# Optimization experiments

Hardware: AMD Instinct MI355X
Metric: run time of the kernel (lower is better)

Reference implementation:

```python
import jax, jax.numpy as jnp
import numpy as np

D_MODEL = 512
D_INNER = 1024   # expand * d_model
D_STATE = 16
D_CONV = 4
DT_RANK = 32     # ceil(d_model / 16)
N_LAYERS = 4
N_PRED_LAYERS = 2
FEAT = 128
LN_EPS = 1e-5


def _ln(x, w, b):
    m = x.mean(-1, keepdims=True)
    v = ((x - m) ** 2).mean(-1, keepdims=True)
    return (x - m) * jax.lax.rsqrt(v + LN_EPS) * w + b


def _silu(x):
    return x * jax.nn.sigmoid(x)


def _causal_conv(x, w, b):
    # depthwise causal conv1d: x (B,L,C), w (C,K), b (C,)
    K = w.shape[1]
    L = x.shape[1]
    xp = jnp.pad(x, ((0, 0), (K - 1, 0), (0, 0)))
    y = b
    for k in range(K):
        y = y + xp[:, k:k + L, :] * w[:, k]
    return y


def _mamba(x, in_w, conv_w, conv_b, xp_w, dt_w, dt_b, Alog, Dp, out_w):
    # x: (B,L,d_model)
    xz = jnp.einsum('bld,ed->ble', x, in_w)          # (B,L,2*d_inner)
    xi, z = jnp.split(xz, 2, axis=-1)
    xc = _silu(_causal_conv(xi, conv_w, conv_b))     # (B,L,d_inner)
    dbc = jnp.einsum('blc,ec->ble', xc, xp_w)        # (B,L,dt_rank+2N)
    dt = dbc[..., :DT_RANK]
    Bm = dbc[..., DT_RANK:DT_RANK + D_STATE]         # (B,L,N)
    Cm = dbc[..., DT_RANK + D_STATE:]                # (B,L,N)
    delta = jax.nn.softplus(jnp.einsum('blr,cr->blc', dt, dt_w) + dt_b)  # (B,L,d_inner)
    A = -jnp.exp(Alog)                               # (d_inner,N), negative
    dA = jnp.exp(delta[..., None] * A)               # (B,L,d_inner,N)
    dBu = delta[..., None] * Bm[:, :, None, :] * xc[..., None]

    def step(h, inp):
        dA_t, dBu_t, C_t = inp
        h = dA_t * h + dBu_t                         # (B,d_inner,N)
        y = jnp.einsum('bcn,bn->bc', h, C_t)
        return h, y

    h0 = jnp.zeros((x.shape[0], D_INNER, D_STATE), x.dtype)
    _, ys = jax.lax.scan(step, h0, (dA.transpose(1, 0, 2, 3),
                                    dBu.transpose(1, 0, 2, 3),
                                    Cm.transpose(1, 0, 2)))
    y = ys.transpose(1, 0, 2) + Dp * xc              # skip connection D*u
    y = y * _silu(z)
    return jnp.einsum('blc,dc->bld', y, out_w)


def _forward(x, inp_w, inp_b, enc_ln_w, enc_ln_b, enc_in_w, enc_conv_w, enc_conv_b,
             enc_xp_w, enc_dt_w, enc_dt_b, enc_Alog, enc_D, enc_out_w,
             fin_ln_w, fin_ln_b, prd_ln_w, prd_ln_b, prd_in_w, prd_conv_w, prd_conv_b,
             prd_xp_w, prd_dt_w, prd_dt_b, prd_Alog, prd_D, prd_out_w,
             prd_nrm_w, prd_nrm_b, prd_proj_w, prd_proj_b):
    # MambaEncoder: input_proj + n_layers pre-norm residual Mamba blocks + final LN
    h = jnp.einsum('blf,df->bld', x, inp_w) + inp_b
    for i in range(N_LAYERS):
        h = h + _mamba(_ln(h, enc_ln_w[i], enc_ln_b[i]),
                       enc_in_w[i], enc_conv_w[i], enc_conv_b[i], enc_xp_w[i],
                       enc_dt_w[i], enc_dt_b[i], enc_Alog[i], enc_D[i], enc_out_w[i])
    ctx = _ln(h, fin_ln_w, fin_ln_b)
    # MambaPredictor: small causal mamba stack + norm + proj
    p = ctx
    for i in range(N_PRED_LAYERS):
        p = p + _mamba(_ln(p, prd_ln_w[i], prd_ln_b[i]),
                       prd_in_w[i], prd_conv_w[i], prd_conv_b[i], prd_xp_w[i],
                       prd_dt_w[i], prd_dt_b[i], prd_Alog[i], prd_D[i], prd_out_w[i])
    p = _ln(p, prd_nrm_w, prd_nrm_b)
    preds = jnp.einsum('bld,ed->ble', p, prd_proj_w) + prd_proj_b
    return preds


def _mamba_params(key, n, scale=0.02):
    ks = jax.random.split(key, 6)
    arange_A = jnp.tile(jnp.log(jnp.arange(1, D_STATE + 1, dtype=jnp.float32)), (n, D_INNER, 1))
    return dict(
        in_w=jax.random.normal(ks[0], (n, 2 * D_INNER, D_MODEL)) * scale,
        conv_w=jax.random.normal(ks[1], (n, D_INNER, D_CONV)) * scale,
        conv_b=jnp.zeros((n, D_INNER)),
        xp_w=jax.random.normal(ks[2], (n, DT_RANK + 2 * D_STATE, D_INNER)) * scale,
        dt_w=jax.random.normal(ks[3], (n, D_INNER, DT_RANK)) * scale,
        dt_b=jnp.full((n, D_INNER), jnp.log(jnp.expm1(0.01))),  # inv-softplus(0.01)
        Alog=arange_A,
        D=jnp.ones((n, D_INNER)),
        out_w=jax.random.normal(ks[4], (n, D_MODEL, D_INNER)) * scale,
    )


def setup_inputs() -> dict:
    key = jax.random.key(0)
    ks = jax.random.split(key, 8)
    enc = _mamba_params(ks[0], N_LAYERS)
    prd = _mamba_params(ks[1], N_PRED_LAYERS)
    return {
        'x': jax.random.normal(ks[2], (2, 1024, FEAT), dtype=jnp.float32),
        'inp_w': jax.random.normal(ks[3], (D_MODEL, FEAT)) * 0.02,
        'inp_b': jnp.zeros((D_MODEL,)),
        'enc_ln_w': jnp.ones((N_LAYERS, D_MODEL)), 'enc_ln_b': jnp.zeros((N_LAYERS, D_MODEL)),
        'enc_in_w': enc['in_w'], 'enc_conv_w': enc['conv_w'], 'enc_conv_b': enc['conv_b'],
        'enc_xp_w': enc['xp_w'], 'enc_dt_w': enc['dt_w'], 'enc_dt_b': enc['dt_b'],
        'enc_Alog': enc['Alog'], 'enc_D': enc['D'], 'enc_out_w': enc['out_w'],
        'fin_ln_w': jnp.ones((D_MODEL,)), 'fin_ln_b': jnp.zeros((D_MODEL,)),
        'prd_ln_w': jnp.ones((N_PRED_LAYERS, D_MODEL)), 'prd_ln_b': jnp.zeros((N_PRED_LAYERS, D_MODEL)),
        'prd_in_w': prd['in_w'], 'prd_conv_w': prd['conv_w'], 'prd_conv_b': prd['conv_b'],
        'prd_xp_w': prd['xp_w'], 'prd_dt_w': prd['dt_w'], 'prd_dt_b': prd['dt_b'],
        'prd_Alog': prd['Alog'], 'prd_D': prd['D'], 'prd_out_w': prd['out_w'],
        'prd_nrm_w': jnp.ones((D_MODEL,)), 'prd_nrm_b': jnp.zeros((D_MODEL,)),
        'prd_proj_w': jax.random.normal(ks[4], (D_MODEL, D_MODEL)) * 0.02,
        'prd_proj_b': jnp.zeros((D_MODEL,)),
    }


def reference(x, inp_w, inp_b, enc_ln_w, enc_ln_b, enc_in_w, enc_conv_w, enc_conv_b,
              enc_xp_w, enc_dt_w, enc_dt_b, enc_Alog, enc_D, enc_out_w,
              fin_ln_w, fin_ln_b, prd_ln_w, prd_ln_b, prd_in_w, prd_conv_w, prd_conv_b,
              prd_xp_w, prd_dt_w, prd_dt_b, prd_Alog, prd_D, prd_out_w,
              prd_nrm_w, prd_nrm_b, prd_proj_w, prd_proj_b):
    return _forward(x, inp_w, inp_b, enc_ln_w, enc_ln_b, enc_in_w, enc_conv_w, enc_conv_b,
                    enc_xp_w, enc_dt_w, enc_dt_b, enc_Alog, enc_D, enc_out_w,
                    fin_ln_w, fin_ln_b, prd_ln_w, prd_ln_b, prd_in_w, prd_conv_w, prd_conv_b,
                    prd_xp_w, prd_dt_w, prd_dt_b, prd_Alog, prd_D, prd_out_w,
                    prd_nrm_w, prd_nrm_b, prd_proj_w, prd_proj_b)
```

## Files before the change

kernel.cpp:

```cpp
#include <hip/hip_runtime.h>
#include <hip/hip_bf16.h>

using bf16 = __hip_bfloat16;
typedef __attribute__((ext_vector_type(8))) short short8;
typedef __attribute__((ext_vector_type(4))) float f32x4;

static constexpr int LB = 2;
static constexpr int LL = 1024;
static constexpr int DM = 512;
static constexpr int DI = 1024;
static constexpr int DSN = 16;
static constexpr int RK = 32;
static constexpr int MR_ROWS = LB * LL;

static constexpr int NCHUNK = 64;
static constexpr int CH = LL / NCHUNK;

__device__ __forceinline__ void gload16(const void* g, void* l) {
    __builtin_amdgcn_global_load_lds(
        (__attribute__((address_space(1))) void*)(g),
        (__attribute__((address_space(3))) void*)(l), 16, 0, 0);
}

struct ConvArgs {
    const float* src[9];
    bf16*        dst[9];
    int          n4[9];
};

__global__ __launch_bounds__(256) void convert_bf16_multi(ConvArgs a) {
    const int s = blockIdx.y;
    const float4* __restrict__ src = (const float4*)a.src[s];
    bf16* __restrict__ dst = a.dst[s];
    const int n4 = a.n4[s];
    for (int i = blockIdx.x * 256 + threadIdx.x; i < n4; i += gridDim.x * 256) {
        float4 v = src[i];
        bf16 t[4] = {__float2bfloat16(v.x), __float2bfloat16(v.y),
                     __float2bfloat16(v.z), __float2bfloat16(v.w)};
        *(uint2*)(dst + (size_t)i * 4) = *(uint2*)t;
    }
}

__global__ __launch_bounds__(256) void transpose_dtw(const float* __restrict__ enc_dtw,
                                                     const float* __restrict__ prd_dtw,
                                                     float* __restrict__ out) {
    const int layer = blockIdx.y;
    const float* src = (layer < 4) ? enc_dtw + (size_t)layer * DI * RK
                                   : prd_dtw + (size_t)(layer - 4) * DI * RK;
    float* dst = out + (size_t)layer * RK * DI;
    const int idx = blockIdx.x * 256 + threadIdx.x;
    const int k = idx >> 10, c = idx & (DI - 1);
    dst[idx] = src[(size_t)c * RK + k];
}

__device__ __forceinline__ void ln_store(float* outrow, int tid, float a, float b) {
    ((float2*)outrow)[tid] = make_float2(a, b);
}
__device__ __forceinline__ void ln_store(bf16* outrow, int tid, float a, float b) {
    __hip_bfloat162 h;
    h.x = __float2bfloat16(a);
    h.y = __float2bfloat16(b);
    ((__hip_bfloat162*)outrow)[tid] = h;
}

template <typename T>
__global__ __launch_bounds__(256) void ln_kernel(const float* __restrict__ x,
                                                 const float* __restrict__ w,
                                                 const float* __restrict__ b,
                                                 T* __restrict__ out) {
    const int row = blockIdx.x;
    const int tid = threadIdx.x;
    const int wid = tid >> 6, lane = tid & 63;
    __shared__ float red[8];

    const float2 v = ((const float2*)(x + (size_t)row * DM))[tid];
    float s = v.x + v.y;
#pragma unroll
    for (int m = 1; m < 64; m <<= 1) s += __shfl_xor(s, m);
    if (lane == 0) red[wid] = s;
    __syncthreads();
    const float mean = (red[0] + red[1] + red[2] + red[3]) * (1.f / DM);
    const float d0 = v.x - mean, d1 = v.y - mean;
    float s2 = d0 * d0 + d1 * d1;
#pragma unroll
    for (int m = 1; m < 64; m <<= 1) s2 += __shfl_xor(s2, m);
    if (lane == 0) red[4 + wid] = s2;
    __syncthreads();
    const float var = (red[4] + red[5] + red[6] + red[7]) * (1.f / DM);
    const float rs = rsqrtf(var + 1e-5f);
    const float2 wv = ((const float2*)w)[tid];
    const float2 bv = ((const float2*)b)[tid];
    ln_store(out + (size_t)row * DM, tid, d0 * rs * wv.x + bv.x, d1 * rs * wv.y + bv.y);
}

template <int BM, int BN, int BK, int EPI>
__global__ __launch_bounds__(256) void gemm_bt(const bf16* __restrict__ A, int lda,
                                               const bf16* __restrict__ B, int ldb,
                                               float* __restrict__ C, int ldc,
                                               int K, const float* __restrict__ bias) {
    static_assert(BK == 64, "layout assumes 128B LDS row");
    static_assert(BM % 32 == 0 && BN % 32 == 0, "wave staging granularity");
    constexpr int MR = (BM / 2) / 16;
    constexpr int NR = (BN / 2) / 16;
    __shared__ __align__(16) char sA[BM * 128];
    __shared__ __align__(16) char sB[BN * 128];

    const int tid = threadIdx.x;
    const int lane = tid & 63, wid = tid >> 6;
    const int wr = wid >> 1, wc = wid & 1;
    const int m0 = blockIdx.y * BM, n0 = blockIdx.x * BN;
    const int kbase = (EPI == 2) ? blockIdx.z * K : 0;

    f32x4 acc[MR][NR] = {};

    const int lrow = lane >> 3;
    const int lcol = (lane & 7) ^ lrow;
    const size_t lda2 = (size_t)lda * 2, ldb2 = (size_t)ldb * 2;
    const char* Ab = (const char*)A + (size_t)(m0 + wid * (BM / 4) + lrow) * lda2
                     + lcol * 16 + (size_t)kbase * 2;
    const char* Bb = (const char*)B + (size_t)(n0 + wid * (BN / 4) + lrow) * ldb2
                     + lcol * 16 + (size_t)kbase * 2;
    char* sAw = sA + wid * (BM / 4) * 128;
    char* sBw = sB + wid * (BN / 4) * 128;

    for (int k0 = 0; k0 < K; k0 += BK) {
#pragma unroll
        for (int i = 0; i < BM / 32; ++i)
            gload16(Ab + (size_t)i * 8 * lda2 + (size_t)k0 * 2, sAw + i * 1024);
#pragma unroll
        for (int i = 0; i < BN / 32; ++i)
            gload16(Bb + (size_t)i * 8 * ldb2 + (size_t)k0 * 2, sBw + i * 1024);
        __syncthreads();
#pragma unroll
        for (int kk = 0; kk < BK; kk += 32) {
            const int kb2 = (kk + (lane >> 4) * 8) * 2;
            short8 af[MR], bfr[NR];
#pragma unroll
            for (int m = 0; m < MR; ++m) {
                const int r = wr * (BM / 2) + m * 16 + (lane & 15);
                af[m] = *(const short8*)(sA + r * 128 + (kb2 ^ ((r & 7) << 4)));
            }
#pragma unroll
            for (int n = 0; n < NR; ++n) {
                const int r = wc * (BN / 2) + n * 16 + (lane & 15);
                bfr[n] = *(const short8*)(sB + r * 128 + (kb2 ^ ((r & 7) << 4)));
            }
#pragma unroll
            for (int m = 0; m < MR; ++m) {
#pragma unroll
                for (int n = 0; n < NR; ++n) {
                    acc[m][n] = __builtin_amdgcn_mfma_f32_16x16x32_bf16(af[m], bfr[n], acc[m][n], 0, 0, 0);
                }
            }
        }
        __syncthreads();
    }

#pragma unroll
    for (int m = 0; m < MR; ++m) {
#pragma unroll
        for (int n = 0; n < NR; ++n) {
            const int col = n0 + wc * (BN / 2) + n * 16 + (lane & 15);
            const float bv = (EPI == 1) ? bias[col] : 0.f;
#pragma unroll
            for (int j = 0; j < 4; ++j) {
                const int row = m0 + wr * (BM / 2) + m * 16 + (lane >> 4) * 4 + j;
                float v = acc[m][n][j] + bv;
                float* p = C + (size_t)row * ldc + col;
                if (EPI == 2) {
                    atomicAdd(p, v);
                } else {
                    if (EPI == 3) v += *p;
                    *p = v;
                }
            }
        }
    }
}

__global__ __launch_bounds__(256) void conv_silu_kernel(const float* __restrict__ xz,
                                                        const float* __restrict__ cw,
                                                        const float* __restrict__ cb,
                                                        float* __restrict__ xc,
                                                        bf16* __restrict__ xc_bf,
                                                        float* __restrict__ dbc_zero) {
    if (blockIdx.x < 128) {
        ((float4*)dbc_zero)[blockIdx.x * 256 + threadIdx.x] = make_float4(0.f, 0.f, 0.f, 0.f);
    }
    const int idx = blockIdx.x * 256 + threadIdx.x;
    const int c = idx & (DI - 1);
    const int r = idx >> 10;
    const int l = r & (LL - 1);
    const float* xi = xz + (size_t)r * (2 * DI) + c;
    const float4 w = *(const float4*)(cw + (size_t)c * 4);
    float acc = cb[c] + w.w * xi[0];
    if (l >= 1) acc += w.z * xi[-(2 * DI)];
    if (l >= 2) acc += w.y * xi[-(4 * DI)];
    if (l >= 3) acc += w.x * xi[-(6 * DI)];
    const float s = acc / (1.f + expf(-acc));
    xc[idx] = s;
    xc_bf[idx] = __float2bfloat16(s);
}

__global__ __launch_bounds__(256) void scan_part1(const float* __restrict__ xc,
                                                  const float* __restrict__ dbc,
                                                  const float* __restrict__ Alog,
                                                  const float* __restrict__ dtw_t,
                                                  const float* __restrict__ dtb,
                                                  float* __restrict__ delta,
                                                  float* __restrict__ psum,
                                                  float* __restrict__ ssum) {
    const int lane = threadIdx.x & 63;
    const int wsub = threadIdx.x >> 6;
    const int c = blockIdx.x * 64 + lane;
    const int chunk = blockIdx.y * 4 + wsub;
    const int b = blockIdx.z;
    const int r0 = b * LL + chunk * CH;

    float wv[RK];
#pragma unroll
    for (int k = 0; k < RK; ++k) wv[k] = dtw_t[(size_t)k * DI + c];
    const float bdt = dtb[c];

    float a2[DSN];
#pragma unroll
    for (int q = 0; q < 4; ++q) {
        const float4 al = *(const float4*)(Alog + (size_t)c * DSN + q * 4);
        a2[q * 4 + 0] = -expf(al.x) * 1.44269504f;
        a2[q * 4 + 1] = -expf(al.y) * 1.44269504f;
        a2[q * 4 + 2] = -expf(al.z) * 1.44269504f;
        a2[q * 4 + 3] = -expf(al.w) * 1.44269504f;
    }

    float h[DSN], P[DSN];
#pragma unroll
    for (int n = 0; n < DSN; ++n) { h[n] = 0.f; P[n] = 1.f; }

    for (int t = 0; t < CH; ++t) {
        const size_t r = r0 + t;
        float acc = bdt;
#pragma unroll
        for (int q = 0; q < RK / 4; ++q) {
            const float4 d4 = *(const float4*)(dbc + r * 64 + q * 4);
            acc = fmaf(d4.x, wv[q * 4 + 0], acc);
            acc = fmaf(d4.y, wv[q * 4 + 1], acc);
            acc = fmaf(d4.z, wv[q * 4 + 2], acc);
            acc = fmaf(d4.w, wv[q * 4 + 3], acc);
        }
        const float d = (acc > 20.f) ? acc : log1pf(expf(acc));
        delta[r * DI + c] = d;

        const float xv = xc[r * DI + c];
        const float dxv = d * xv;
        float Bv[DSN];
#pragma unroll
        for (int q = 0; q < 4; ++q)
            *(float4*)&Bv[q * 4] = *(const float4*)(dbc + r * 64 + 32 + q * 4);
#pragma unroll
        for (int n = 0; n < DSN; ++n) {
            const float dA = exp2f(d * a2[n]);
            h[n] = fmaf(dA, h[n], dxv * Bv[n]);
            P[n] *= dA;
        }
    }

    const size_t obase = ((size_t)(b * NCHUNK + chunk) * DSN) * DI + c;
#pragma unroll
    for (int n = 0; n < DSN; ++n) {
        psum[obase + (size_t)n * DI] = P[n];
        ssum[obase + (size_t)n * DI] = h[n];
    }
}

__global__ __launch_bounds__(256) void scan_combine(float* __restrict__ psum,
                                                    const float* __restrict__ ssum) {
    const int lane = threadIdx.x & 63;
    const int idx = blockIdx.y * 4 + (threadIdx.x >> 6);
    const int b = idx >> 4, n = idx & 15;
    const int c = blockIdx.x * 64 + lane;
    const size_t base = ((size_t)(b * NCHUNK) * DSN + n) * DI + c;
    const size_t stride = (size_t)DSN * DI;

    float h = 0.f;
    for (int j0 = 0; j0 < NCHUNK; j0 += 8) {
        float Pv[8], Sv[8];
#pragma unroll
        for (int u = 0; u < 8; ++u) {
            Pv[u] = psum[base + (j0 + u) * stride];
            Sv[u] = ssum[base + (j0 + u) * stride];
        }
#pragma unroll
        for (int u = 0; u < 8; ++u) {
            psum[base + (j0 + u) * stride] = h;
            h = fmaf(Pv[u], h, Sv[u]);
        }
    }
}

__global__ __launch_bounds__(256) void scan_part3(const float* __restrict__ delta,
                                                  const float* __restrict__ xc,
                                                  const float* __restrict__ xz,
                                                  const float* __restrict__ dbc,
                                                  const float* __restrict__ Alog,
                                                  const float* __restrict__ Dp,
                                                  const float* __restrict__ hin,
                                                  bf16* __restrict__ yg) {
    const int lane = threadIdx.x & 63;
    const int wsub = threadIdx.x >> 6;
    const int c = blockIdx.x * 64 + lane;
    const int chunk = blockIdx.y * 4 + wsub;
    const int b = blockIdx.z;
    const int r0 = b * LL + chunk * CH;

    float a2[DSN];
#pragma unroll
    for (int q = 0; q < 4; ++q) {
        const float4 al = *(const float4*)(Alog + (size_t)c * DSN + q * 4);
        a2[q * 4 + 0] = -expf(al.x) * 1.44269504f;
        a2[q * 4 + 1] = -expf(al.y) * 1.44269504f;
        a2[q * 4 + 2] = -expf(al.z) * 1.44269504f;
        a2[q * 4 + 3] = -expf(al.w) * 1.44269504f;
    }
    const float dp = Dp[c];

    float h[DSN];
    const size_t hbase = ((size_t)(b * NCHUNK + chunk) * DSN) * DI + c;
#pragma unroll
    for (int n = 0; n < DSN; ++n) h[n] = hin[hbase + (size_t)n * DI];

    for (int t = 0; t < CH; ++t) {
        const size_t r = r0 + t;
        const float d  = delta[r * DI + c];
        const float xv = xc[r * DI + c];
        const float zv = xz[r * (2 * DI) + DI + c];
        const float dxv = d * xv;
        float Bv[DSN], Cv[DSN];
#pragma unroll
        for (int q = 0; q < 4; ++q) {
            *(float4*)&Bv[q * 4] = *(const float4*)(dbc + r * 64 + 32 + q * 4);
            *(float4*)&Cv[q * 4] = *(const float4*)(dbc + r * 64 + 48 + q * 4);
        }
        float y0 = 0.f, y1 = 0.f, y2 = 0.f, y3 = 0.f;
#pragma unroll
        for (int q = 0; q < 4; ++q) {
            {
                const float dA = exp2f(d * a2[q * 4 + 0]);
                h[q * 4 + 0] = fmaf(dA, h[q * 4 + 0], dxv * Bv[q * 4 + 0]);
                y0 = fmaf(h[q * 4 + 0], Cv[q * 4 + 0], y0);
            }
            {
                const float dA = exp2f(d * a2[q * 4 + 1]);
                h[q * 4 + 1] = fmaf(dA, h[q * 4 + 1], dxv * Bv[q * 4 + 1]);
                y1 = fmaf(h[q * 4 + 1], Cv[q * 4 + 1], y1);
            }
            {
                const float dA = exp2f(d * a2[q * 4 + 2]);
                h[q * 4 + 2] = fmaf(dA, h[q * 4 + 2], dxv * Bv[q * 4 + 2]);
                y2 = fmaf(h[q * 4 + 2], Cv[q * 4 + 2], y2);
            }
            {
                const float dA = exp2f(d * a2[q * 4 + 3]);
                h[q * 4 + 3] = fmaf(dA, h[q * 4 + 3], dxv * Bv[q * 4 + 3]);
                y3 = fmaf(h[q * 4 + 3], Cv[q * 4 + 3], y3);
            }
        }
        const float y = (y0 + y1) + (y2 + y3);
        const float zs = zv / (1.f + expf(-zv));
        yg[r * DI + c] = __float2bfloat16((y + dp * xv) * zs);
    }
}

static void run_mamba_layer(hipStream_t stream, float* resid,
                            const float* ln_w, const float* ln_b,
                            const bf16* inw_bf,
                            const float* conv_w, const float* conv_b,
                            const bf16* xpw_bf,
                            const float* dtw_t, const float* dt_b,
                            const float* Alog, const float* Dp,
                            const bf16* outw_bf,
                            bf16* ln_bf, float* xz, float* xc, bf16* xc_bf,
                            float* dbc, float* delta,
                            float* psum, float* ssum, bf16* yg_bf) {
    ln_kernel<bf16><<<MR_ROWS, 256, 0, stream>>>(resid, ln_w, ln_b, ln_bf);
    gemm_bt<64, 64, 64, 0><<<dim3(2 * DI / 64, MR_ROWS / 64), 256, 0, stream>>>(
        ln_bf, DM, inw_bf, DM, xz, 2 * DI, DM, nullptr);
    conv_silu_kernel<<<MR_ROWS * DI / 256, 256, 0, stream>>>(xz, conv_w, conv_b, xc, xc_bf, dbc);
    gemm_bt<32, 64, 64, 2><<<dim3(1, MR_ROWS / 32, 4), 256, 0, stream>>>(
        xc_bf, DI, xpw_bf, DI, dbc, 64, DI / 4, nullptr);
    scan_part1<<<dim3(DI / 64, NCHUNK / 4, LB), 256, 0, stream>>>(
        xc, dbc, Alog, dtw_t, dt_b, delta, psum, ssum);
    scan_combine<<<dim3(DI / 64, (LB * DSN) / 4), 256, 0, stream>>>(psum, ssum);
    scan_part3<<<dim3(DI / 64, NCHUNK / 4, LB), 256, 0, stream>>>(
        delta, xc, xz, dbc, Alog, Dp, psum, yg_bf);
    gemm_bt<32, 64, 64, 3><<<dim3(DM / 64, MR_ROWS / 32), 256, 0, stream>>>(
        yg_bf, DI, outw_bf, DI, resid, DM, DI, nullptr);
}

extern "C" void kernel_launch(void* const* d_in, const int* in_sizes, int n_in,
                              void* d_out, int out_size, void* d_ws, size_t ws_size,
                              hipStream_t stream) {
    const float* x         = (const float*)d_in[0];
    const float* inp_w     = (const float*)d_in[1];
    const float* inp_b     = (const float*)d_in[2];
    const float* enc_ln_w  = (const float*)d_in[3];
    const float* enc_ln_b  = (const float*)d_in[4];
    const float* enc_in_w  = (const float*)d_in[5];
    const float* enc_conv_w= (const float*)d_in[6];
    const float* enc_conv_b= (const float*)d_in[7];
    const float* enc_xp_w  = (const float*)d_in[8];
    const float* enc_dt_w  = (const float*)d_in[9];
    const float* enc_dt_b  = (const float*)d_in[10];
    const float* enc_Alog  = (const float*)d_in[11];
    const float* enc_D     = (const float*)d_in[12];
    const float* enc_out_w = (const float*)d_in[13];
    const float* fin_ln_w  = (const float*)d_in[14];
    const float* fin_ln_b  = (const float*)d_in[15];
    const float* prd_ln_w  = (const float*)d_in[16];
    const float* prd_ln_b  = (const float*)d_in[17];
    const float* prd_in_w  = (const float*)d_in[18];
    const float* prd_conv_w= (const float*)d_in[19];
    const float* prd_conv_b= (const float*)d_in[20];
    const float* prd_xp_w  = (const float*)d_in[21];
    const float* prd_dt_w  = (const float*)d_in[22];
    const float* prd_dt_b  = (const float*)d_in[23];
    const float* prd_Alog  = (const float*)d_in[24];
    const float* prd_D     = (const float*)d_in[25];
    const float* prd_out_w = (const float*)d_in[26];
    const float* prd_nrm_w = (const float*)d_in[27];
    const float* prd_nrm_b = (const float*)d_in[28];
    const float* prd_proj_w= (const float*)d_in[29];
    const float* prd_proj_b= (const float*)d_in[30];

    char* wp = (char*)d_ws;
    auto carve = [&](size_t elems, size_t esz) {
        void* p = (void*)wp;
        wp += (elems * esz + 255) & ~(size_t)255;
        return p;
    };
    bf16* x_bf     = (bf16*)carve((size_t)MR_ROWS * 128, 2);
    bf16* inpw_bf  = (bf16*)carve((size_t)DM * 128, 2);
    bf16* einw_bf  = (bf16*)carve(4ull * 2 * DI * DM, 2);
    bf16* expw_bf  = (bf16*)carve(4ull * 64 * DI, 2);
    bf16* eoutw_bf = (bf16*)carve(4ull * DM * DI, 2);
    bf16* pinw_bf  = (bf16*)carve(2ull * 2 * DI * DM, 2);
    bf16* pxpw_bf  = (bf16*)carve(2ull * 64 * DI, 2);
    bf16* poutw_bf = (bf16*)carve(2ull * DM * DI, 2);
    bf16* projw_bf = (bf16*)carve((size_t)DM * DM, 2);
    float* dtwt    = (float*)carve(6ull * RK * DI, 4);
    float* hbuf    = (float*)carve((size_t)MR_ROWS * DM, 4);
    float* pbuf    = (float*)carve((size_t)MR_ROWS * DM, 4);
    bf16* ln_bf    = (bf16*)carve((size_t)MR_ROWS * DM, 2);
    float* xz      = (float*)carve((size_t)MR_ROWS * 2 * DI, 4);
    float* xc      = (float*)carve((size_t)MR_ROWS * DI, 4);
    bf16* xc_bf    = (bf16*)carve((size_t)MR_ROWS * DI, 2);
    float* dbc     = (float*)carve((size_t)MR_ROWS * 64, 4);
    float* delta   = (float*)carve((size_t)MR_ROWS * DI, 4);
    float* psum    = (float*)carve((size_t)LB * NCHUNK * DSN * DI, 4);
    float* ssum    = (float*)carve((size_t)LB * NCHUNK * DSN * DI, 4);
    bf16* yg_bf    = (bf16*)carve((size_t)MR_ROWS * DI, 2);

    ConvArgs ca;
    const float* csrc[9] = {x, inp_w, enc_in_w, enc_xp_w, enc_out_w,
                            prd_in_w, prd_xp_w, prd_out_w, prd_proj_w};
    bf16* cdst[9] = {x_bf, inpw_bf, einw_bf, expw_bf, eoutw_bf,
                     pinw_bf, pxpw_bf, poutw_bf, projw_bf};
    const int cn[9] = {MR_ROWS * 128, DM * 128, 4 * 2 * DI * DM, 4 * 64 * DI, 4 * DM * DI,
                       2 * 2 * DI * DM, 2 * 64 * DI, 2 * DM * DI, DM * DM};
    for (int i = 0; i < 9; ++i) { ca.src[i] = csrc[i]; ca.dst[i] = cdst[i]; ca.n4[i] = cn[i] / 4; }
    convert_bf16_multi<<<dim3(128, 9), 256, 0, stream>>>(ca);
    transpose_dtw<<<dim3(RK * DI / 256, 6), 256, 0, stream>>>(enc_dt_w, prd_dt_w, dtwt);

    gemm_bt<32, 64, 64, 1><<<dim3(DM / 64, MR_ROWS / 32), 256, 0, stream>>>(
        x_bf, 128, inpw_bf, 128, hbuf, DM, 128, inp_b);

    for (int i = 0; i < 4; ++i) {
        run_mamba_layer(stream, hbuf,
                        enc_ln_w + (size_t)i * DM, enc_ln_b + (size_t)i * DM,
                        einw_bf + (size_t)i * 2 * DI * DM,
                        enc_conv_w + (size_t)i * DI * 4, enc_conv_b + (size_t)i * DI,
                        expw_bf + (size_t)i * 64 * DI,
                        dtwt + (size_t)i * RK * DI, enc_dt_b + (size_t)i * DI,
                        enc_Alog + (size_t)i * DI * DSN, enc_D + (size_t)i * DI,
                        eoutw_bf + (size_t)i * DM * DI,
                        ln_bf, xz, xc, xc_bf, dbc, delta, psum, ssum, yg_bf);
    }

    ln_kernel<float><<<MR_ROWS, 256, 0, stream>>>(hbuf, fin_ln_w, fin_ln_b, pbuf);

    for (int i = 0; i < 2; ++i) {
        run_mamba_layer(stream, pbuf,
                        prd_ln_w + (size_t)i * DM, prd_ln_b + (size_t)i * DM,
                        pinw_bf + (size_t)i * 2 * DI * DM,
                        prd_conv_w + (size_t)i * DI * 4, prd_conv_b + (size_t)i * DI,
                        pxpw_bf + (size_t)i * 64 * DI,
                        dtwt + (size_t)(4 + i) * RK * DI, prd_dt_b + (size_t)i * DI,
                        prd_Alog + (size_t)i * DI * DSN, prd_D + (size_t)i * DI,
                        poutw_bf + (size_t)i * DM * DI,
                        ln_bf, xz, xc, xc_bf, dbc, delta, psum, ssum, yg_bf);
    }

    ln_kernel<bf16><<<MR_ROWS, 256, 0, stream>>>(pbuf, prd_nrm_w, prd_nrm_b, ln_bf);
    gemm_bt<32, 64, 64, 1><<<dim3(DM / 64, MR_ROWS / 32), 256, 0, stream>>>(
        ln_bf, DM, projw_bf, DM, (float*)d_out, DM, DM, prd_proj_b);

    (void)in_sizes; (void)n_in; (void)out_size; (void)ws_size;
}
```

Measured before the change: 652.3 us.

## Fuse conv+x_proj via MFMA, store xz in bf16, recompute delta in scan

The in-projection GEMM now writes xz as bf16 instead of fp32. The causal conv+SiLU is fused with the x_proj GEMM into one MFMA kernel that atomically accumulates dbc, and the separate K-split GEMM launch is removed. Delta is no longer stored; scan_part3 recomputes it from dbc and the transposed dt weights, and the fp32 xc and delta buffers are dropped. LayerNorm now handles one row per wave without LDS reductions and also does the dbc zeroing. This cuts memory traffic and launch count in exchange for extra recompute and lower precision on intermediates.

```diff
diff --git a/kernel.cpp b/kernel.cpp
--- a/kernel.cpp
+++ b/kernel.cpp
@@ -53,44 +53,58 @@
     dst[idx] = src[(size_t)c * RK + k];
 }
 
-__device__ __forceinline__ void ln_store(float* outrow, int tid, float a, float b) {
-    ((float2*)outrow)[tid] = make_float2(a, b);
-}
-__device__ __forceinline__ void ln_store(bf16* outrow, int tid, float a, float b) {
-    __hip_bfloat162 h;
-    h.x = __float2bfloat16(a);
-    h.y = __float2bfloat16(b);
-    ((__hip_bfloat162*)outrow)[tid] = h;
+__device__ __forceinline__ void ln_store8(float* outrow, int lane,
+                                          const float* v) {
+    float4 a = {v[0], v[1], v[2], v[3]}, b = {v[4], v[5], v[6], v[7]};
+    ((float4*)outrow)[lane] = a;
+    ((float4*)outrow)[lane + 64] = b;
+}
+__device__ __forceinline__ void ln_store8(bf16* outrow, int lane,
+                                          const float* v) {
+    bf16 t0[4] = {__float2bfloat16(v[0]), __float2bfloat16(v[1]),
+                  __float2bfloat16(v[2]), __float2bfloat16(v[3])};
+    bf16 t1[4] = {__float2bfloat16(v[4]), __float2bfloat16(v[5]),
+                  __float2bfloat16(v[6]), __float2bfloat16(v[7])};
+    ((uint2*)outrow)[lane] = *(uint2*)t0;
+    ((uint2*)outrow)[lane + 64] = *(uint2*)t1;
 }
 
 template <typename T>
 __global__ __launch_bounds__(256) void ln_kernel(const float* __restrict__ x,
                                                  const float* __restrict__ w,
                                                  const float* __restrict__ b,
-                                                 T* __restrict__ out) {
-    const int row = blockIdx.x;
-    const int tid = threadIdx.x;
-    const int wid = tid >> 6, lane = tid & 63;
-    __shared__ float red[8];
-
-    const float2 v = ((const float2*)(x + (size_t)row * DM))[tid];
-    float s = v.x + v.y;
+                                                 T* __restrict__ out,
+                                                 float* __restrict__ dbc_zero) {
+    if (dbc_zero != nullptr && blockIdx.x < 128) {
+        ((float4*)dbc_zero)[blockIdx.x * 256 + threadIdx.x] =
+            make_float4(0.f, 0.f, 0.f, 0.f);
+    }
+    const int wid = threadIdx.x >> 6, lane = threadIdx.x & 63;
+    const int row = blockIdx.x * 4 + wid;
+    const float4* xr = (const float4*)(x + (size_t)row * DM);
+    const float4 v0 = xr[lane], v1 = xr[lane + 64];
+
+    float s = (v0.x + v0.y + v0.z + v0.w) + (v1.x + v1.y + v1.z + v1.w);
 #pragma unroll
     for (int m = 1; m < 64; m <<= 1) s += __shfl_xor(s, m);
-    if (lane == 0) red[wid] = s;
-    __syncthreads();
-    const float mean = (red[0] + red[1] + red[2] + red[3]) * (1.f / DM);
-    const float d0 = v.x - mean, d1 = v.y - mean;
-    float s2 = d0 * d0 + d1 * d1;
+    const float mean = s * (1.f / DM);
+
+    float d[8] = {v0.x - mean, v0.y - mean, v0.z - mean, v0.w - mean,
+                  v1.x - mean, v1.y - mean, v1.z - mean, v1.w - mean};
+    float s2 = 0.f;
+#pragma unroll
+    for (int q = 0; q < 8; ++q) s2 += d[q] * d[q];
 #pragma unroll
     for (int m = 1; m < 64; m <<= 1) s2 += __shfl_xor(s2, m);
-    if (lane == 0) red[4 + wid] = s2;
-    __syncthreads();
-    const float var = (red[4] + red[5] + red[6] + red[7]) * (1.f / DM);
-    const float rs = rsqrtf(var + 1e-5f);
-    const float2 wv = ((const float2*)w)[tid];
-    const float2 bv = ((const float2*)b)[tid];
-    ln_store(out + (size_t)row * DM, tid, d0 * rs * wv.x + bv.x, d1 * rs * wv.y + bv.y);
+    const float rs = rsqrtf(s2 * (1.f / DM) + 1e-5f);
+
+    const float4 w0 = ((const float4*)w)[lane], w1 = ((const float4*)w)[lane + 64];
+    const float4 b0 = ((const float4*)b)[lane], b1 = ((const float4*)b)[lane + 64];
+    float o[8] = {d[0] * rs * w0.x + b0.x, d[1] * rs * w0.y + b0.y,
+                  d[2] * rs * w0.z + b0.z, d[3] * rs * w0.w + b0.w,
+                  d[4] * rs * w1.x + b1.x, d[5] * rs * w1.y + b1.y,
+                  d[6] * rs * w1.z + b1.z, d[7] * rs * w1.w + b1.w};
+    ln_store8(out + (size_t)row * DM, lane, o);
 }
 
 template <int BM, int BN, int BK, int EPI>
@@ -166,48 +180,94 @@
             for (int j = 0; j < 4; ++j) {
                 const int row = m0 + wr * (BM / 2) + m * 16 + (lane >> 4) * 4 + j;
                 float v = acc[m][n][j] + bv;
-                float* p = C + (size_t)row * ldc + col;
-                if (EPI == 2) {
-                    atomicAdd(p, v);
+                if (EPI == 4) {
+                    ((bf16*)C)[(size_t)row * ldc + col] = __float2bfloat16(v);
                 } else {
-                    if (EPI == 3) v += *p;
-                    *p = v;
+                    float* p = C + (size_t)row * ldc + col;
+                    if (EPI == 2) {
+                        atomicAdd(p, v);
+                    } else {
+                        if (EPI == 3) v += *p;
+                        *p = v;
+                    }
                 }
             }
         }
     }
 }
 
-__global__ __launch_bounds__(256) void conv_silu_kernel(const float* __restrict__ xz,
-                                                        const float* __restrict__ cw,
-                                                        const float* __restrict__ cb,
-                                                        float* __restrict__ xc,
-                                                        bf16* __restrict__ xc_bf,
-                                                        float* __restrict__ dbc_zero) {
-    if (blockIdx.x < 128) {
-        ((float4*)dbc_zero)[blockIdx.x * 256 + threadIdx.x] = make_float4(0.f, 0.f, 0.f, 0.f);
-    }
-    const int idx = blockIdx.x * 256 + threadIdx.x;
-    const int c = idx & (DI - 1);
-    const int r = idx >> 10;
-    const int l = r & (LL - 1);
-    const float* xi = xz + (size_t)r * (2 * DI) + c;
-    const float4 w = *(const float4*)(cw + (size_t)c * 4);
-    float acc = cb[c] + w.w * xi[0];
-    if (l >= 1) acc += w.z * xi[-(2 * DI)];
-    if (l >= 2) acc += w.y * xi[-(4 * DI)];
-    if (l >= 3) acc += w.x * xi[-(6 * DI)];
-    const float s = acc / (1.f + expf(-acc));
-    xc[idx] = s;
-    xc_bf[idx] = __float2bfloat16(s);
-}
-
-__global__ __launch_bounds__(256) void scan_part1(const float* __restrict__ xc,
+__global__ __launch_bounds__(256) void conv_mfma(const bf16* __restrict__ xzb,
+                                                 const float* __restrict__ cw,
+                                                 const float* __restrict__ cb,
+                                                 const bf16* __restrict__ xpw,
+                                                 bf16* __restrict__ xc_bf,
+                                                 float* __restrict__ dbc) {
+    const int c0 = blockIdx.x * 64;
+    const int r0 = blockIdx.y * 64;
+    const int tid = threadIdx.x, lane = tid & 63, wid = tid >> 6;
+    __shared__ __align__(16) char sX[64 * 128];
+    __shared__ __align__(16) char sW[64 * 128];
+
+    const int lrow = lane >> 3, lcol = (lane & 7) ^ lrow;
+    {
+        const char* Wb = (const char*)xpw + (size_t)(wid * 16 + lrow) * (DI * 2)
+                         + c0 * 2 + lcol * 16;
+        char* sWw = sW + wid * 16 * 128;
+        gload16(Wb, sWw);
+        gload16(Wb + 8 * (DI * 2), sWw + 8 * 128);
+    }
+
+    const int c = lane;
+    const int rgrp = wid;
+    const float4 w = *(const float4*)(cw + (size_t)(c0 + c) * 4);
+    const float cbv = cb[c0 + c];
+#pragma unroll
+    for (int i = 0; i < 16; ++i) {
+        const int r = rgrp + i * 4;
+        const int rowg = r0 + r;
+        const int bstart = (rowg >> 10) << 10;
+        const bf16* xi = xzb + (size_t)rowg * (2 * DI) + c0 + c;
+        float acc = cbv + w.w * __bfloat162float(xi[0]);
+        if (rowg - 1 >= bstart) acc += w.z * __bfloat162float(xi[-(2 * DI)]);
+        if (rowg - 2 >= bstart) acc += w.y * __bfloat162float(xi[-(4 * DI)]);
+        if (rowg - 3 >= bstart) acc += w.x * __bfloat162float(xi[-(6 * DI)]);
+        const float s = acc / (1.f + expf(-acc));
+        const bf16 sb = __float2bfloat16(s);
+        xc_bf[(size_t)rowg * DI + c0 + c] = sb;
+        *(bf16*)(sX + r * 128 + ((c * 2) ^ ((r & 7) << 4))) = sb;
+    }
+    __syncthreads();
+
+    f32x4 acc[4] = {};
+    const int kb2 = (lane >> 4) * 16;
+#pragma unroll
+    for (int kk = 0; kk < 2; ++kk) {
+        const int kbyte = kk * 64 + kb2;
+        const int ra = wid * 16 + (lane & 15);
+        const short8 af = *(const short8*)(sX + ra * 128 + (kbyte ^ ((ra & 7) << 4)));
+#pragma unroll
+        for (int n = 0; n < 4; ++n) {
+            const int re = n * 16 + (lane & 15);
+            const short8 bfr = *(const short8*)(sW + re * 128 + (kbyte ^ ((re & 7) << 4)));
+            acc[n] = __builtin_amdgcn_mfma_f32_16x16x32_bf16(af, bfr, acc[n], 0, 0, 0);
+        }
+    }
+#pragma unroll
+    for (int n = 0; n < 4; ++n) {
+        const int col = n * 16 + (lane & 15);
+#pragma unroll
+        for (int j = 0; j < 4; ++j) {
+            const int row = r0 + wid * 16 + (lane >> 4) * 4 + j;
+            atomicAdd(&dbc[(size_t)row * 64 + col], acc[n][j]);
+        }
+    }
+}
+
+__global__ __launch_bounds__(256) void scan_part1(const bf16* __restrict__ xcb,
                                                   const float* __restrict__ dbc,
                                                   const float* __restrict__ Alog,
                                                   const float* __restrict__ dtw_t,
                                                   const float* __restrict__ dtb,
-                                                  float* __restrict__ delta,
                                                   float* __restrict__ psum,
                                                   float* __restrict__ ssum) {
     const int lane = threadIdx.x & 63;
@@ -248,9 +308,8 @@
             acc = fmaf(d4.w, wv[q * 4 + 3], acc);
         }
         const float d = (acc > 20.f) ? acc : log1pf(expf(acc));
-        delta[r * DI + c] = d;
-
-        const float xv = xc[r * DI + c];
+
+        const float xv = __bfloat162float(xcb[r * DI + c]);
         const float dxv = d * xv;
         float Bv[DSN];
 #pragma unroll
@@ -297,11 +356,12 @@
     }
 }
 
-__global__ __launch_bounds__(256) void scan_part3(const float* __restrict__ delta,
-                                                  const float* __restrict__ xc,
-                                                  const float* __restrict__ xz,
+__global__ __launch_bounds__(256) void scan_part3(const bf16* __restrict__ xcb,
+                                                  const bf16* __restrict__ xzb,
                                                   const float* __restrict__ dbc,
                                                   const float* __restrict__ Alog,
+                                                  const float* __restrict__ dtw_t,
+                                                  const float* __restrict__ dtb,
                                                   const float* __restrict__ Dp,
                                                   const float* __restrict__ hin,
                                                   bf16* __restrict__ yg) {
@@ -312,6 +372,11 @@
     const int b = blockIdx.z;
     const int r0 = b * LL + chunk * CH;
 
+    float wv[RK];
+#pragma unroll
+    for (int k = 0; k < RK; ++k) wv[k] = dtw_t[(size_t)k * DI + c];
+    const float bdt = dtb[c];
+
     float a2[DSN];
 #pragma unroll
     for (int q = 0; q < 4; ++q) {
@@ -330,9 +395,19 @@
 
     for (int t = 0; t < CH; ++t) {
         const size_t r = r0 + t;
-        const float d  = delta[r * DI + c];
-        const float xv = xc[r * DI + c];
-        const float zv = xz[r * (2 * DI) + DI + c];
+        float acc = bdt;
+#pragma unroll
+        for (int q = 0; q < RK / 4; ++q) {
+            const float4 d4 = *(const float4*)(dbc + r * 64 + q * 4);
+            acc = fmaf(d4.x, wv[q * 4 + 0], acc);
+            acc = fmaf(d4.y, wv[q * 4 + 1], acc);
+            acc = fmaf(d4.z, wv[q * 4 + 2], acc);
+            acc = fmaf(d4.w, wv[q * 4 + 3], acc);
+        }
+        const float d = (acc > 20.f) ? acc : log1pf(expf(acc));
+
+        const float xv = __bfloat162float(xcb[r * DI + c]);
+        const float zv = __bfloat162float(xzb[r * (2 * DI) + DI + c]);
         const float dxv = d * xv;
         float Bv[DSN], Cv[DSN];
 #pragma unroll
@@ -378,20 +453,19 @@
                             const float* dtw_t, const float* dt_b,
                             const float* Alog, const float* Dp,
                             const bf16* outw_bf,
-                            bf16* ln_bf, float* xz, float* xc, bf16* xc_bf,
-                            float* dbc, float* delta,
+                            bf16* ln_bf, bf16* xzb, bf16* xc_bf,
+                            float* dbc,
                             float* psum, float* ssum, bf16* yg_bf) {
-    ln_kernel<bf16><<<MR_ROWS, 256, 0, stream>>>(resid, ln_w, ln_b, ln_bf);
-    gemm_bt<64, 64, 64, 0><<<dim3(2 * DI / 64, MR_ROWS / 64), 256, 0, stream>>>(
-        ln_bf, DM, inw_bf, DM, xz, 2 * DI, DM, nullptr);
-    conv_silu_kernel<<<MR_ROWS * DI / 256, 256, 0, stream>>>(xz, conv_w, conv_b, xc, xc_bf, dbc);
-    gemm_bt<32, 64, 64, 2><<<dim3(1, MR_ROWS / 32, 4), 256, 0, stream>>>(
-        xc_bf, DI, xpw_bf, DI, dbc, 64, DI / 4, nullptr);
+    ln_kernel<bf16><<<MR_ROWS / 4, 256, 0, stream>>>(resid, ln_w, ln_b, ln_bf, dbc);
+    gemm_bt<64, 64, 64, 4><<<dim3(2 * DI / 64, MR_ROWS / 64), 256, 0, stream>>>(
+        ln_bf, DM, inw_bf, DM, (float*)xzb, 2 * DI, DM, nullptr);
+    conv_mfma<<<dim3(DI / 64, MR_ROWS / 64), 256, 0, stream>>>(
+        xzb, conv_w, conv_b, xpw_bf, xc_bf, dbc);
     scan_part1<<<dim3(DI / 64, NCHUNK / 4, LB), 256, 0, stream>>>(
-        xc, dbc, Alog, dtw_t, dt_b, delta, psum, ssum);
+        xc_bf, dbc, Alog, dtw_t, dt_b, psum, ssum);
     scan_combine<<<dim3(DI / 64, (LB * DSN) / 4), 256, 0, stream>>>(psum, ssum);
     scan_part3<<<dim3(DI / 64, NCHUNK / 4, LB), 256, 0, stream>>>(
-        delta, xc, xz, dbc, Alog, Dp, psum, yg_bf);
+        xc_bf, xzb, dbc, Alog, dtw_t, dt_b, Dp, psum, yg_bf);
     gemm_bt<32, 64, 64, 3><<<dim3(DM / 64, MR_ROWS / 32), 256, 0, stream>>>(
         yg_bf, DI, outw_bf, DI, resid, DM, DI, nullptr);
 }
@@ -450,11 +524,9 @@
     float* hbuf    = (float*)carve((size_t)MR_ROWS * DM, 4);
     float* pbuf    = (float*)carve((size_t)MR_ROWS * DM, 4);
     bf16* ln_bf    = (bf16*)carve((size_t)MR_ROWS * DM, 2);
-    float* xz      = (float*)carve((size_t)MR_ROWS * 2 * DI, 4);
-    float* xc      = (float*)carve((size_t)MR_ROWS * DI, 4);
+    bf16* xzb      = (bf16*)carve((size_t)MR_ROWS * 2 * DI, 2);
     bf16* xc_bf    = (bf16*)carve((size_t)MR_ROWS * DI, 2);
     float* dbc     = (float*)carve((size_t)MR_ROWS * 64, 4);
-    float* delta   = (float*)carve((size_t)MR_ROWS * DI, 4);
     float* psum    = (float*)carve((size_t)LB * NCHUNK * DSN * DI, 4);
     float* ssum    = (float*)carve((size_t)LB * NCHUNK * DSN * DI, 4);
     bf16* yg_bf    = (bf16*)carve((size_t)MR_ROWS * DI, 2);
@@ -482,10 +554,10 @@
                         dtwt + (size_t)i * RK * DI, enc_dt_b + (size_t)i * DI,
                         enc_Alog + (size_t)i * DI * DSN, enc_D + (size_t)i * DI,
                         eoutw_bf + (size_t)i * DM * DI,
-                        ln_bf, xz, xc, xc_bf, dbc, delta, psum, ssum, yg_bf);
-    }
-
-    ln_kernel<float><<<MR_ROWS, 256, 0, stream>>>(hbuf, fin_ln_w, fin_ln_b, pbuf);
+                        ln_bf, xzb, xc_bf, dbc, psum, ssum, yg_bf);
+    }
+
+    ln_kernel<float><<<MR_ROWS / 4, 256, 0, stream>>>(hbuf, fin_ln_w, fin_ln_b, pbuf, nullptr);
 
     for (int i = 0; i < 2; ++i) {
         run_mamba_layer(stream, pbuf,
@@ -496,10 +568,10 @@
                         dtwt + (size_t)(4 + i) * RK * DI, prd_dt_b + (size_t)i * DI,
                         prd_Alog + (size_t)i * DI * DSN, prd_D + (size_t)i * DI,
                         poutw_bf + (size_t)i * DM * DI,
-                        ln_bf, xz, xc, xc_bf, dbc, delta, psum, ssum, yg_bf);
-    }
-
-    ln_kernel<bf16><<<MR_ROWS, 256, 0, stream>>>(pbuf, prd_nrm_w, prd_nrm_b, ln_bf);
+                        ln_bf, xzb, xc_bf, dbc, psum, ssum, yg_bf);
+    }
+
+    ln_kernel<bf16><<<MR_ROWS / 4, 256, 0, stream>>>(pbuf, prd_nrm_w, prd_nrm_b, ln_bf, nullptr);
     gemm_bt<32, 64, 64, 1><<<dim3(DM / 64, MR_ROWS / 32), 256, 0, stream>>>(
         ln_bf, DM, projw_bf, DM, (float*)d_out, DM, DM, prd_proj_b);
 
```

Measured after the change: 693.7 us. 1.06x slower.
